# Kernel tuning notes

Hardware: AMD Instinct MI355X
Metric: run time of the kernel (lower is better)

## Reference

```python
import jax, jax.numpy as jnp
import numpy as np

EMBED_DIM = 1024
NUM_HEADS = 16
HEAD_DIM = EMBED_DIM // NUM_HEADS
B, T = 4, 1024
NEG = -1.0e9
LN_EPS = 1e-5


def setup_inputs() -> dict:
    key = jax.random.key(0)
    ks = jax.random.split(key, 13)
    s = 1.0 / np.sqrt(EMBED_DIM)
    return {
        "query": jax.random.normal(ks[0], (B, T, EMBED_DIM), jnp.float32),
        "key": jax.random.normal(ks[1], (B, T, EMBED_DIM), jnp.float32),
        "value": jax.random.normal(ks[2], (B, T, EMBED_DIM), jnp.float32),
        "mask": jax.random.randint(ks[3], (B, 1, T, T), 0, 2, jnp.int32),
        "Wq": jax.random.normal(ks[4], (EMBED_DIM, EMBED_DIM), jnp.float32) * s,
        "bq": jnp.zeros((EMBED_DIM,), jnp.float32),
        "Wk": jax.random.normal(ks[5], (EMBED_DIM, EMBED_DIM), jnp.float32) * s,
        "bk": jnp.zeros((EMBED_DIM,), jnp.float32),
        "Wv": jax.random.normal(ks[6], (EMBED_DIM, EMBED_DIM), jnp.float32) * s,
        "bv": jnp.zeros((EMBED_DIM,), jnp.float32),
        "Wo": jax.random.normal(ks[7], (EMBED_DIM, EMBED_DIM), jnp.float32) * s,
        "bo": jnp.zeros((EMBED_DIM,), jnp.float32),
        "gamma": jnp.ones((EMBED_DIM,), jnp.float32),
        "beta": jnp.zeros((EMBED_DIM,), jnp.float32),
    }


def _split_heads(x):
    # (B, T, E) -> (B, H, T, D)
    b, t, _ = x.shape
    return x.reshape(b, t, NUM_HEADS, HEAD_DIM).transpose(0, 2, 1, 3)


def _mha(query, key, value, mask, Wq, bq, Wk, bk, Wv, bv, Wo, bo, gamma, beta,
         temperature=1.0):
    q = _split_heads(query @ Wq.T + bq)
    k = _split_heads(key @ Wk.T + bk)
    v = _split_heads(value @ Wv.T + bv)
    # scores: (B, H, T, T)
    scale = jnp.sqrt(jnp.float32(HEAD_DIM)) * temperature
    scores = jnp.einsum("bhqd,bhkd->bhqk", q, k) / scale
    scores = jnp.where(mask == 0, NEG, scores)
    scores = scores - jnp.max(scores, axis=-1, keepdims=True)
    # temperature >= 0.01 in this config, so the low-temperature hard-cutoff
    # branch is skipped (matches torch's Python-level `if temperature < 0.01`).
    scores = jnp.nan_to_num(scores, nan=0.0, posinf=1.0e9, neginf=-1.0e9)
    attn = jax.nn.softmax(scores, axis=-1)
    # eval mode: dropout is identity (self.training is False)
    out = jnp.einsum("bhqk,bhkd->bhqd", attn, v)  # (B, H, T, D)
    out = out.transpose(0, 2, 1, 3).reshape(query.shape[0], query.shape[1], EMBED_DIM)
    out = out @ Wo.T + bo
    # layer norm over embed_dim
    mu = jnp.mean(out, axis=-1, keepdims=True)
    var = jnp.mean(jnp.square(out - mu), axis=-1, keepdims=True)
    out = (out - mu) * jax.lax.rsqrt(var + LN_EPS) * gamma + beta
    return out


def reference(query, key, value, mask, Wq, bq, Wk, bk, Wv, bv, Wo, bo, gamma, beta):
    return _mha(query, key, value, mask, Wq, bq, Wk, bk, Wv, bv, Wo, bo, gamma, beta)
```

## Files before the change

### kernel.cpp

```cpp
#include <hip/hip_runtime.h>
#include <cmath>

#define T_SEQ 1024
#define EMB   1024
#define NH    16
#define HD    64
#define NB    4
#define BQ    64
#define BK    64

#define QSCALE 0.18033688011112042f
#define BIAS2  -1.44269504e9f

using frag8   = __attribute__((ext_vector_type(8))) short;
using f32x4   = __attribute__((ext_vector_type(4))) float;
using short4v = __attribute__((ext_vector_type(4))) short;
using short8v = __attribute__((ext_vector_type(8))) short;

__device__ inline short f2bf(float f) {
    union { float f; unsigned u; } x; x.f = f;
    unsigned r = (x.u + 0x7FFFu + ((x.u >> 16) & 1u)) >> 16;
    return (short)r;
}
__device__ inline short f2bf_rhu(float f) {
    union { float f; unsigned u; } x; x.f = f;
    return (short)((x.u + 0x8000u) >> 16);
}
__device__ inline float bf2f(unsigned short u) {
    union { unsigned u; float f; } x; x.u = ((unsigned)u) << 16;
    return x.f;
}

__device__ inline void glds16(const short* g, short* l) {
    __builtin_amdgcn_global_load_lds(
        (const __attribute__((address_space(1))) void*)g,
        (__attribute__((address_space(3))) void*)l, 16, 0, 0);
}

struct ConvArgs { const float* src[7]; short* dst[7]; int n8[7]; };

__global__ __launch_bounds__(256) void convert_bf16(ConvArgs a) {
    const int y = blockIdx.y;
    const int t = blockIdx.x * 256 + threadIdx.x;
    if (t >= a.n8[y]) return;
    const float4* s = (const float4*)a.src[y];
    const float4 v0 = s[t * 2], v1 = s[t * 2 + 1];
    short8v o;
    o[0] = f2bf(v0.x); o[1] = f2bf(v0.y); o[2] = f2bf(v0.z); o[3] = f2bf(v0.w);
    o[4] = f2bf(v1.x); o[5] = f2bf(v1.y); o[6] = f2bf(v1.z); o[7] = f2bf(v1.w);
    *(short8v*)&a.dst[y][t * 8] = o;
}

__global__ __launch_bounds__(256) void convert_mask(
    const int* __restrict__ mask, short* __restrict__ dst)
{
    const int wave = threadIdx.x >> 6, lane = threadIdx.x & 63;
    const int tile = blockIdx.x * 4 + wave;
    const int bb   = tile >> 12;
    const int q16  = (tile >> 6) & 63;
    const int k16  = tile & 63;
    const int qrow = lane >> 2;
    const int col4 = (lane & 3) * 4;
    const int4 mv = *(const int4*)&mask[((size_t)bb * T_SEQ + q16 * 16 + qrow) * T_SEQ
                                        + k16 * 16 + col4];
    const short BB = f2bf(BIAS2);
    short4v o;
    o[0] = mv.x ? (short)0 : BB;
    o[1] = mv.y ? (short)0 : BB;
    o[2] = mv.z ? (short)0 : BB;
    o[3] = mv.w ? (short)0 : BB;
    *(short4v*)&dst[(size_t)tile * 256 + qrow * 16 + col4] = o;
}

struct GemmB { const short* A; const short* W; const float* bias; short* out; float scale; };
struct QkvArgs { GemmB g[3]; };

template <int MODE>
__device__ inline void gemm_core(const short* __restrict__ A,
                                 const short* __restrict__ W,
                                 const float* __restrict__ bias,
                                 float scale,
                                 short* __restrict__ outS,
                                 float* __restrict__ outF,
                                 int m0, int n0)
{
    __shared__ short As[2][128 * 32];
    __shared__ short Bs[2][128 * 32];

    const int tid  = threadIdx.x;
    const int wave = tid >> 6;
    const int lane = tid & 63;
    const int quad = lane >> 4;
    const int lm   = lane & 15;
    const int wr   = wave >> 1;
    const int wc   = wave & 1;
    const int K    = EMB;

    const int G0 = wave * 64 + lane, G1 = G0 + 256;
    const short* aSrc0 = A + (size_t)(m0 + (G0 >> 2)) * K + (G0 & 3) * 8;
    const short* aSrc1 = A + (size_t)(m0 + (G1 >> 2)) * K + (G1 & 3) * 8;
    const short* bSrc0 = W + (size_t)(n0 + (G0 >> 2)) * K + (G0 & 3) * 8;
    const short* bSrc1 = W + (size_t)(n0 + (G1 >> 2)) * K + (G1 & 3) * 8;
    short* aDst0 = &As[0][wave * 512];
    short* aDst1 = &As[0][2048 + wave * 512];
    short* bDst0 = &Bs[0][wave * 512];
    short* bDst1 = &Bs[0][2048 + wave * 512];

    f32x4 acc[4][4];
#pragma unroll
    for (int i = 0; i < 4; ++i)
#pragma unroll
        for (int j = 0; j < 4; ++j) acc[i][j] = (f32x4){0.f, 0.f, 0.f, 0.f};

    for (int kk = 0; kk < K; kk += 64) {
        __syncthreads();
        glds16(aSrc0 + kk,      aDst0);
        glds16(aSrc1 + kk,      aDst1);
        glds16(bSrc0 + kk,      bDst0);
        glds16(bSrc1 + kk,      bDst1);
        glds16(aSrc0 + kk + 32, aDst0 + 4096);
        glds16(aSrc1 + kk + 32, aDst1 + 4096);
        glds16(bSrc0 + kk + 32, bDst0 + 4096);
        glds16(bSrc1 + kk + 32, bDst1 + 4096);
        __syncthreads();

#pragma unroll
        for (int p = 0; p < 2; ++p) {
            frag8 aF[4], bF[4];
#pragma unroll
            for (int i = 0; i < 4; ++i)
                aF[i] = *(const frag8*)&As[p][(wr * 64 + i * 16 + lm) * 32 + quad * 8];
#pragma unroll
            for (int j = 0; j < 4; ++j)
                bF[j] = *(const frag8*)&Bs[p][(wc * 64 + j * 16 + lm) * 32 + quad * 8];
#pragma unroll
            for (int i = 0; i < 4; ++i)
#pragma unroll
                for (int j = 0; j < 4; ++j)
                    acc[i][j] = __builtin_amdgcn_mfma_f32_16x16x32_bf16(
                        aF[i], bF[j], acc[i][j], 0, 0, 0);
        }
    }

#pragma unroll
    for (int i = 0; i < 4; ++i)
#pragma unroll
        for (int j = 0; j < 4; ++j) {
            const int n = n0 + wc * 64 + j * 16 + lm;
            const float bv = bias[n];
#pragma unroll
            for (int rr = 0; rr < 4; ++rr) {
                const int m = m0 + wr * 64 + i * 16 + quad * 4 + rr;
                const float val = (acc[i][j][rr] + bv) * scale;
                if (MODE == 0) {
                    outF[((size_t)(m >> 4) * 64 + (n >> 4)) * 256 +
                         rr * 64 + quad * 16 + lm] = val;
                } else {
                    const int bb = m >> 10, tt = m & 1023;
                    const int h = n >> 6,  d  = n & 63;
                    const size_t bh = (size_t)bb * NH + h;
                    if (MODE == 1) {
                        outS[((bh * 64 + (tt >> 4)) * 8 + (d >> 3)) * 128 +
                             (tt & 15) * 8 + (d & 7)] = f2bf(val);
                    } else {
                        outS[((((bh * 16 + (tt >> 6)) * 2 + ((tt >> 5) & 1)) * 4 +
                              (d >> 4)) * 4 + ((tt >> 3) & 3)) * 128 +
                             (d & 15) * 8 + (tt & 7)] = f2bf(val);
                    }
                }
            }
        }
}

__global__ __launch_bounds__(256, 3) void gemm_qkv(QkvArgs args) {
    const int id = blockIdx.x + 8 * blockIdx.y + 256 * blockIdx.z;
    const int a  = id & 7;
    const int k2 = id >> 3;
    const int nb = k2 & 7;
    const int c  = k2 >> 3;
    const int pair = a * 12 + c;
    const int mb = pair & 31;
    const int zb = pair >> 5;
    const GemmB g = args.g[zb];
    if (zb < 2) gemm_core<1>(g.A, g.W, g.bias, g.scale, g.out, nullptr, mb * 128, nb * 128);
    else        gemm_core<2>(g.A, g.W, g.bias, g.scale, g.out, nullptr, mb * 128, nb * 128);
}

__global__ __launch_bounds__(256, 3) void gemm_wo(const short* __restrict__ A,
                                                  const short* __restrict__ W,
                                                  const float* __restrict__ bias,
                                                  float* __restrict__ out) {
    const int id = blockIdx.x + 8 * blockIdx.y;
    const int a  = id & 7;
    const int k2 = id >> 3;
    const int nb = k2 & 7;
    const int c  = k2 >> 3;
    const int mb = a * 4 + c;
    gemm_core<0>(A, W, bias, 1.0f, nullptr, out, mb * 128, nb * 128);
}

__global__ __launch_bounds__(256, 4) void flash_attn_mfma(
    const short* __restrict__ qf_, const short* __restrict__ kf_,
    const short* __restrict__ vf_, const short* __restrict__ mf_,
    short* __restrict__ out)
{
    __shared__ short Pl[4][2][16][72];

    const int tid  = threadIdx.x;
    const int wave = tid >> 6;
    const int lane = tid & 63;
    const int quad = lane >> 4;
    const int lm   = lane & 15;

    const int id  = blockIdx.x;
    const int xcd = id & 7;
    const int idx = id >> 3;
    const int bh_i = xcd * 8 + (idx >> 4);
    const int b  = bh_i >> 4, h = bh_i & 15;
    const int q0 = (idx & 15) * BQ;
    const size_t bh = (size_t)bh_i;

    const short* qb_ = qf_ + (bh * 64 + (q0 >> 4) + wave) * 1024;
    const frag8 qfa = *(const frag8*)&qb_[(quad * 16 + lm) * 8];
    const frag8 qfb = *(const frag8*)&qb_[((quad + 4) * 16 + lm) * 8];

    const short* mrow = mf_ + ((size_t)b * 64 + (q0 >> 4) + wave) * (64 * 256)
                        + lm * 16 + quad * 4;

    f32x4 of[4];
#pragma unroll
    for (int dc = 0; dc < 4; ++dc) of[dc] = (f32x4){0.f, 0.f, 0.f, 0.f};
    float lsum = 0.f;

    for (int kt2 = 0; kt2 < T_SEQ / BK; ++kt2) {
        const int pp = kt2 & 1;

        frag8 vf[2][4];
        const short* vbase = vf_ + (bh * 16 + kt2) * 4096;
#pragma unroll
        for (int kh2 = 0; kh2 < 2; ++kh2)
#pragma unroll
            for (int dc = 0; dc < 4; ++dc)
                vf[kh2][dc] = *(const frag8*)
                    &vbase[((kh2 * 4 + dc) * 4 + quad) * 128 + lm * 8];

        short4v mb[4];
#pragma unroll
        for (int kc = 0; kc < 4; ++kc)
            mb[kc] = *(const short4v*)&mrow[(kt2 * 4 + kc) * 256];

        f32x4 s[4];
#pragma unroll
        for (int kc = 0; kc < 4; ++kc) {
            const short* kbase = kf_ + (bh * 64 + kt2 * 4 + kc) * 1024;
            const frag8 kfa = *(const frag8*)&kbase[(quad * 16 + lm) * 8];
            const frag8 kfb = *(const frag8*)&kbase[((quad + 4) * 16 + lm) * 8];
            f32x4 a = (f32x4){ bf2f((unsigned short)mb[kc][0]),
                               bf2f((unsigned short)mb[kc][1]),
                               bf2f((unsigned short)mb[kc][2]),
                               bf2f((unsigned short)mb[kc][3]) };
            a = __builtin_amdgcn_mfma_f32_16x16x32_bf16(kfa, qfa, a, 0, 0, 0);
            a = __builtin_amdgcn_mfma_f32_16x16x32_bf16(kfb, qfb, a, 0, 0, 0);
            s[kc] = a;
        }

#pragma unroll
        for (int kc = 0; kc < 4; ++kc) {
            float p0 = exp2f(s[kc][0]), p1 = exp2f(s[kc][1]);
            float p2 = exp2f(s[kc][2]), p3 = exp2f(s[kc][3]);
            lsum += (p0 + p1) + (p2 + p3);
            short4v pk;
            pk[0] = f2bf_rhu(p0); pk[1] = f2bf_rhu(p1);
            pk[2] = f2bf_rhu(p2); pk[3] = f2bf_rhu(p3);
            *(short4v*)&Pl[wave][pp][lm][kc * 16 + quad * 4] = pk;
        }

        const frag8 pfa = *(const frag8*)&Pl[wave][pp][lm][quad * 8];
        const frag8 pfb = *(const frag8*)&Pl[wave][pp][lm][32 + quad * 8];
#pragma unroll
        for (int dc = 0; dc < 4; ++dc) {
            of[dc] = __builtin_amdgcn_mfma_f32_16x16x32_bf16(vf[0][dc], pfa, of[dc], 0, 0, 0);
            of[dc] = __builtin_amdgcn_mfma_f32_16x16x32_bf16(vf[1][dc], pfb, of[dc], 0, 0, 0);
        }
    }

    lsum += __shfl_xor(lsum, 16);
    lsum += __shfl_xor(lsum, 32);
    const float inv = 1.0f / lsum;

    short* ob = out + ((size_t)b * T_SEQ + q0 + wave * 16 + lm) * EMB + h * HD;
#pragma unroll
    for (int dc = 0; dc < 4; ++dc) {
        short4v o4;
#pragma unroll
        for (int rr = 0; rr < 4; ++rr) o4[rr] = f2bf(of[dc][rr] * inv);
        *(short4v*)&ob[dc * 16 + quad * 4] = o4;
    }
}

__global__ __launch_bounds__(256) void layernorm_k(
    const float* __restrict__ x, const float* __restrict__ gamma,
    const float* __restrict__ beta, float* __restrict__ out)
{
    __shared__ float ws1[4], ws2[4];
    const int tid = threadIdx.x;
    const int row = blockIdx.x;
    const int m16 = row >> 4, rr = row & 3, qd = (row >> 2) & 3;

    const float4 v = *(const float4*)&x[((size_t)m16 * 64 + (tid >> 2)) * 256 +
                                        rr * 64 + qd * 16 + (tid & 3) * 4];
    float s  = v.x + v.y + v.z + v.w;
    float ss = v.x * v.x + v.y * v.y + v.z * v.z + v.w * v.w;
#pragma unroll
    for (int off = 32; off > 0; off >>= 1) {
        s  += __shfl_down(s, off);
        ss += __shfl_down(ss, off);
    }
    if ((tid & 63) == 0) { ws1[tid >> 6] = s; ws2[tid >> 6] = ss; }
    __syncthreads();
    if (tid == 0) {
        const float a = ws1[0] + ws1[1] + ws1[2] + ws1[3];
        const float bsum = ws2[0] + ws2[1] + ws2[2] + ws2[3];
        const float mu = a * (1.0f / EMB);
        const float var = bsum * (1.0f / EMB) - mu * mu;
        ws1[0] = mu;
        ws2[0] = rsqrtf(var + 1e-5f);
    }
    __syncthreads();
    const float mu = ws1[0], rstd = ws2[0];

    const float4 g = *(const float4*)&gamma[tid * 4];
    const float4 bt = *(const float4*)&beta[tid * 4];
    float4 r;
    r.x = (v.x - mu) * rstd * g.x + bt.x;
    r.y = (v.y - mu) * rstd * g.y + bt.y;
    r.z = (v.z - mu) * rstd * g.z + bt.z;
    r.w = (v.w - mu) * rstd * g.w + bt.w;
    *(float4*)&out[(size_t)row * EMB + tid * 4] = r;
}

extern "C" void kernel_launch(void* const* d_in, const int* in_sizes, int n_in,
                              void* d_out, int out_size, void* d_ws, size_t ws_size,
                              hipStream_t stream) {
    const float* query = (const float*)d_in[0];
    const float* key_i = (const float*)d_in[1];
    const float* value = (const float*)d_in[2];
    const int*   mask  = (const int*)d_in[3];
    const float* Wq = (const float*)d_in[4];
    const float* bq = (const float*)d_in[5];
    const float* Wk = (const float*)d_in[6];
    const float* bk = (const float*)d_in[7];
    const float* Wv = (const float*)d_in[8];
    const float* bv = (const float*)d_in[9];
    const float* Wo = (const float*)d_in[10];
    const float* bo = (const float*)d_in[11];
    const float* gamma = (const float*)d_in[12];
    const float* beta  = (const float*)d_in[13];

    const size_t SZ = (size_t)NB * T_SEQ * EMB;
    const size_t WZ = (size_t)EMB * EMB;
    short* sws = (short*)d_ws;
    short* q_bf  = sws;
    short* k_bf  = sws + SZ;
    short* v_bf  = sws + 2 * SZ;
    short* w_bf  = sws + 3 * SZ;
    short* qh    = sws + 4 * SZ;
    short* kh    = sws + 5 * SZ;
    short* vh    = sws + 6 * SZ;
    short* maskb = sws + 7 * SZ;
    short* attnb = q_bf;
    float* projb = (float*)(sws + SZ);

    ConvArgs ca;
    ca.src[0] = query; ca.dst[0] = q_bf;          ca.n8[0] = (int)(SZ / 8);
    ca.src[1] = key_i; ca.dst[1] = k_bf;          ca.n8[1] = (int)(SZ / 8);
    ca.src[2] = value; ca.dst[2] = v_bf;          ca.n8[2] = (int)(SZ / 8);
    ca.src[3] = Wq;    ca.dst[3] = w_bf;          ca.n8[3] = (int)(WZ / 8);
    ca.src[4] = Wk;    ca.dst[4] = w_bf + WZ;     ca.n8[4] = (int)(WZ / 8);
    ca.src[5] = Wv;    ca.dst[5] = w_bf + 2 * WZ; ca.n8[5] = (int)(WZ / 8);
    ca.src[6] = Wo;    ca.dst[6] = w_bf + 3 * WZ; ca.n8[6] = (int)(WZ / 8);
    convert_bf16<<<dim3((SZ / 8 + 255) / 256, 7), 256, 0, stream>>>(ca);

    convert_mask<<<dim3(NB * 64 * 64 / 4), 256, 0, stream>>>(mask, maskb);

    QkvArgs qa;
    qa.g[0] = { q_bf, w_bf,          bq, qh, QSCALE };
    qa.g[1] = { k_bf, w_bf + WZ,     bk, kh, 1.0f };
    qa.g[2] = { v_bf, w_bf + 2 * WZ, bv, vh, 1.0f };
    gemm_qkv<<<dim3(EMB / 128, NB * T_SEQ / 128, 3), 256, 0, stream>>>(qa);

    flash_attn_mfma<<<dim3(T_SEQ / BQ * NH * NB), 256, 0, stream>>>(qh, kh, vh, maskb, attnb);

    gemm_wo<<<dim3(EMB / 128, NB * T_SEQ / 128), 256, 0, stream>>>(
        attnb, w_bf + 3 * WZ, bo, projb);

    layernorm_k<<<dim3(NB * T_SEQ), 256, 0, stream>>>(projb, gamma, beta, (float*)d_out);
}
```

Measured before the change: 259.4 us.

## Split attention key range across two wave groups and pack P in registers

The attention block grows to 512 threads. Two groups of four waves each process half of the key tiles, and the second group's partial outputs and row sums are reduced through shared memory at the end. The V layout written by the QKV GEMM is permuted so the bf16-packed probabilities can feed the PV MFMA straight from registers via v_cvt_pk_bf16_f32, which drops the LDS round trip for P. The PV MFMAs are also wrapped in s_setprio. This adds a block-wide sync and more register pressure per thread.

```diff
diff --git a/kernel.cpp b/kernel.cpp
--- a/kernel.cpp
+++ b/kernel.cpp
@@ -22,13 +22,14 @@
     unsigned r = (x.u + 0x7FFFu + ((x.u >> 16) & 1u)) >> 16;
     return (short)r;
 }
-__device__ inline short f2bf_rhu(float f) {
-    union { float f; unsigned u; } x; x.f = f;
-    return (short)((x.u + 0x8000u) >> 16);
-}
 __device__ inline float bf2f(unsigned short u) {
     union { unsigned u; float f; } x; x.u = ((unsigned)u) << 16;
     return x.f;
+}
+__device__ inline int cvt_pk_bf16(float lo, float hi) {
+    int r;
+    asm("v_cvt_pk_bf16_f32 %0, %1, %2" : "=v"(r) : "v"(lo), "v"(hi));
+    return r;
 }
 
 __device__ inline void glds16(const short* g, short* l) {
@@ -164,8 +165,8 @@
                              (tt & 15) * 8 + (d & 7)] = f2bf(val);
                     } else {
                         outS[((((bh * 16 + (tt >> 6)) * 2 + ((tt >> 5) & 1)) * 4 +
-                              (d >> 4)) * 4 + ((tt >> 3) & 3)) * 128 +
-                             (d & 15) * 8 + (tt & 7)] = f2bf(val);
+                              (d >> 4)) * 4 + ((tt >> 2) & 3)) * 128 +
+                             (d & 15) * 8 + (((tt & 16) >> 2) | (tt & 3))] = f2bf(val);
                     }
                 }
             }
@@ -199,18 +200,20 @@
     gemm_core<0>(A, W, bias, 1.0f, nullptr, out, mb * 128, nb * 128);
 }
 
-__global__ __launch_bounds__(256, 4) void flash_attn_mfma(
+__global__ __launch_bounds__(512, 8) void flash_attn_mfma(
     const short* __restrict__ qf_, const short* __restrict__ kf_,
     const short* __restrict__ vf_, const short* __restrict__ mf_,
     short* __restrict__ out)
 {
-    __shared__ short Pl[4][2][16][72];
+    __shared__ float Osh[4][17][64];
 
     const int tid  = threadIdx.x;
     const int wave = tid >> 6;
     const int lane = tid & 63;
     const int quad = lane >> 4;
     const int lm   = lane & 15;
+    const int wq   = wave & 3;
+    const int wk   = wave >> 2;
 
     const int id  = blockIdx.x;
     const int xcd = id & 7;
@@ -220,11 +223,11 @@
     const int q0 = (idx & 15) * BQ;
     const size_t bh = (size_t)bh_i;
 
-    const short* qb_ = qf_ + (bh * 64 + (q0 >> 4) + wave) * 1024;
+    const short* qb_ = qf_ + (bh * 64 + (q0 >> 4) + wq) * 1024;
     const frag8 qfa = *(const frag8*)&qb_[(quad * 16 + lm) * 8];
     const frag8 qfb = *(const frag8*)&qb_[((quad + 4) * 16 + lm) * 8];
 
-    const short* mrow = mf_ + ((size_t)b * 64 + (q0 >> 4) + wave) * (64 * 256)
+    const short* mrow = mf_ + ((size_t)b * 64 + (q0 >> 4) + wq) * (64 * 256)
                         + lm * 16 + quad * 4;
 
     f32x4 of[4];
@@ -232,17 +235,17 @@
     for (int dc = 0; dc < 4; ++dc) of[dc] = (f32x4){0.f, 0.f, 0.f, 0.f};
     float lsum = 0.f;
 
-    for (int kt2 = 0; kt2 < T_SEQ / BK; ++kt2) {
-        const int pp = kt2 & 1;
-
-        frag8 vf[2][4];
+    for (int kt = 0; kt < 8; ++kt) {
+        const int kt2 = wk * 8 + kt;
+
+        frag8 vfr[2][4];
         const short* vbase = vf_ + (bh * 16 + kt2) * 4096;
 #pragma unroll
-        for (int kh2 = 0; kh2 < 2; ++kh2)
+        for (int hf = 0; hf < 2; ++hf)
 #pragma unroll
             for (int dc = 0; dc < 4; ++dc)
-                vf[kh2][dc] = *(const frag8*)
-                    &vbase[((kh2 * 4 + dc) * 4 + quad) * 128 + lm * 8];
+                vfr[hf][dc] = *(const frag8*)
+                    &vbase[((hf * 4 + dc) * 4 + quad) * 128 + lm * 8];
 
         short4v mb[4];
 #pragma unroll
@@ -264,37 +267,56 @@
             s[kc] = a;
         }
 
+        float p[4][4];
 #pragma unroll
         for (int kc = 0; kc < 4; ++kc) {
-            float p0 = exp2f(s[kc][0]), p1 = exp2f(s[kc][1]);
-            float p2 = exp2f(s[kc][2]), p3 = exp2f(s[kc][3]);
-            lsum += (p0 + p1) + (p2 + p3);
-            short4v pk;
-            pk[0] = f2bf_rhu(p0); pk[1] = f2bf_rhu(p1);
-            pk[2] = f2bf_rhu(p2); pk[3] = f2bf_rhu(p3);
-            *(short4v*)&Pl[wave][pp][lm][kc * 16 + quad * 4] = pk;
-        }
-
-        const frag8 pfa = *(const frag8*)&Pl[wave][pp][lm][quad * 8];
-        const frag8 pfb = *(const frag8*)&Pl[wave][pp][lm][32 + quad * 8];
+            p[kc][0] = exp2f(s[kc][0]); p[kc][1] = exp2f(s[kc][1]);
+            p[kc][2] = exp2f(s[kc][2]); p[kc][3] = exp2f(s[kc][3]);
+            lsum += (p[kc][0] + p[kc][1]) + (p[kc][2] + p[kc][3]);
+        }
+
+        union { int i[4]; frag8 f; } ua, ub;
+        ua.i[0] = cvt_pk_bf16(p[0][0], p[0][1]);
+        ua.i[1] = cvt_pk_bf16(p[0][2], p[0][3]);
+        ua.i[2] = cvt_pk_bf16(p[1][0], p[1][1]);
+        ua.i[3] = cvt_pk_bf16(p[1][2], p[1][3]);
+        ub.i[0] = cvt_pk_bf16(p[2][0], p[2][1]);
+        ub.i[1] = cvt_pk_bf16(p[2][2], p[2][3]);
+        ub.i[2] = cvt_pk_bf16(p[3][0], p[3][1]);
+        ub.i[3] = cvt_pk_bf16(p[3][2], p[3][3]);
+
+        __builtin_amdgcn_s_setprio(1);
 #pragma unroll
         for (int dc = 0; dc < 4; ++dc) {
-            of[dc] = __builtin_amdgcn_mfma_f32_16x16x32_bf16(vf[0][dc], pfa, of[dc], 0, 0, 0);
-            of[dc] = __builtin_amdgcn_mfma_f32_16x16x32_bf16(vf[1][dc], pfb, of[dc], 0, 0, 0);
-        }
-    }
-
-    lsum += __shfl_xor(lsum, 16);
-    lsum += __shfl_xor(lsum, 32);
-    const float inv = 1.0f / lsum;
-
-    short* ob = out + ((size_t)b * T_SEQ + q0 + wave * 16 + lm) * EMB + h * HD;
-#pragma unroll
-    for (int dc = 0; dc < 4; ++dc) {
-        short4v o4;
-#pragma unroll
-        for (int rr = 0; rr < 4; ++rr) o4[rr] = f2bf(of[dc][rr] * inv);
-        *(short4v*)&ob[dc * 16 + quad * 4] = o4;
+            of[dc] = __builtin_amdgcn_mfma_f32_16x16x32_bf16(vfr[0][dc], ua.f, of[dc], 0, 0, 0);
+            of[dc] = __builtin_amdgcn_mfma_f32_16x16x32_bf16(vfr[1][dc], ub.f, of[dc], 0, 0, 0);
+        }
+        __builtin_amdgcn_s_setprio(0);
+    }
+
+    if (wk) {
+#pragma unroll
+        for (int c = 0; c < 16; ++c) Osh[wq][c][lane] = of[c >> 2][c & 3];
+        Osh[wq][16][lane] = lsum;
+    }
+    __syncthreads();
+    if (!wk) {
+#pragma unroll
+        for (int c = 0; c < 16; ++c) of[c >> 2][c & 3] += Osh[wq][c][lane];
+        lsum += Osh[wq][16][lane];
+
+        lsum += __shfl_xor(lsum, 16);
+        lsum += __shfl_xor(lsum, 32);
+        const float inv = 1.0f / lsum;
+
+        short* ob = out + ((size_t)b * T_SEQ + q0 + wq * 16 + lm) * EMB + h * HD;
+#pragma unroll
+        for (int dc = 0; dc < 4; ++dc) {
+            short4v o4;
+#pragma unroll
+            for (int rr = 0; rr < 4; ++rr) o4[rr] = f2bf(of[dc][rr] * inv);
+            *(short4v*)&ob[dc * 16 + quad * 4] = o4;
+        }
     }
 }
 
@@ -389,7 +411,7 @@
     qa.g[2] = { v_bf, w_bf + 2 * WZ, bv, vh, 1.0f };
     gemm_qkv<<<dim3(EMB / 128, NB * T_SEQ / 128, 3), 256, 0, stream>>>(qa);
 
-    flash_attn_mfma<<<dim3(T_SEQ / BQ * NH * NB), 256, 0, stream>>>(qh, kh, vh, maskb, attnb);
+    flash_attn_mfma<<<dim3(T_SEQ / BQ * NH * NB), 512, 0, stream>>>(qh, kh, vh, maskb, attnb);
 
     gemm_wo<<<dim3(EMB / 128, NB * T_SEQ / 128), 256, 0, stream>>>(
         attnb, w_bf + 3 * WZ, bo, projb);
```

Result: slower. 353.6 us (+36.3%).
